# Optimization experiments

Measured on AMD Instinct MI355X. Metric: run time of the kernel, lower is better.

## Reference

```python
import jax, jax.numpy as jnp
import numpy as np


def setup_inputs() -> dict:
    key = jax.random.key(0)
    ks = jax.random.split(key, 7)
    B, C, L, A = 8, 1024, 2048, 128
    x = jax.random.normal(ks[0], (B, C, L), dtype=jnp.float32)
    Wk = jax.random.normal(ks[1], (A, C), dtype=jnp.float32) * (1.0 / np.sqrt(C))
    bk = jax.random.normal(ks[2], (A,), dtype=jnp.float32) * 0.01
    Wq = jax.random.normal(ks[3], (A, C), dtype=jnp.float32) * (1.0 / np.sqrt(C))
    bq = jax.random.normal(ks[4], (A,), dtype=jnp.float32) * 0.01
    Wp = jax.random.normal(ks[5], (C, C), dtype=jnp.float32) * (1.0 / np.sqrt(C))
    bp = jax.random.normal(ks[6], (C,), dtype=jnp.float32) * 0.01
    return {"x": x, "Wk": Wk, "bk": bk, "Wq": Wq, "bq": bq, "Wp": Wp, "bp": bp}


def reference(x, Wk, bk, Wq, bq, Wp, bp):
    # x: [B, C, L]; 1x1 Conv1d == pointwise linear over channel dim
    keys = jnp.einsum('bcl,ac->bal', x, Wk) + bk[None, :, None]      # [B, A, L]
    queries = jnp.einsum('bcl,ac->bal', x, Wq) + bq[None, :, None]   # [B, A, L]
    values = jnp.einsum('bal,bam->blm', keys, queries)               # keys^T @ queries -> [B, L, L]
    seqlen = x.shape[2]
    # NOTE: source uses seqlen ** 1 / 2 which is seqlen/2 due to Python precedence
    attn = jax.nn.softmax(values / (seqlen / 2.0), axis=-1)          # [B, L, L]
    out = jnp.einsum('bcl,blm->bcm', x, attn)                        # x @ attn -> [B, C, L]
    out = jnp.einsum('bcm,dc->bdm', out, Wp) + bp[None, :, None]     # output projection
    return out
```

## Files before the change

kernel.cpp:

```cpp
#include <hip/hip_runtime.h>
#include <hip/hip_bf16.h>

typedef __hip_bfloat16 bf16;
typedef __attribute__((ext_vector_type(8))) short bfrag8;
typedef __attribute__((ext_vector_type(8))) int intx8;
typedef __attribute__((ext_vector_type(4))) float floatx4;


__device__ __forceinline__ unsigned char f2fp8(float f) {
    f = fminf(fmaxf(f, -448.f), 448.f);
    return (unsigned char)(__builtin_amdgcn_cvt_pk_fp8_f32(f, f, 0, false) & 0xFF);
}

__device__ __forceinline__ void async_copy16(const void* g, void* lds) {
    __builtin_amdgcn_global_load_lds(
        (const __attribute__((address_space(1))) unsigned int*)g,
        (__attribute__((address_space(3))) unsigned int*)lds, 16, 0, 0);
}

template<int BIASMODE, int OUTKIND, bool EXPZ, bool MFAST>
__global__ __launch_bounds__(256)
void gemm128(const bf16* __restrict__ Ag, long sAb, int lda,
             const bf16* __restrict__ Bg, long sBb, int ldb,
             void* __restrict__ Cg, long sCb, int ldc,
             const float* __restrict__ scl, const float* __restrict__ b2,
             float* __restrict__ Zp, int K, int logfast)
{
    __shared__ unsigned short As[128 * 64];
    __shared__ unsigned short Bs[128 * 64];

    const int lin = blockIdx.x;
    const int bz  = lin & 7;
    const int s   = lin >> 3;
    const int msk = (1 << logfast) - 1;
    int mT, nT;
    if (MFAST) { mT = s & msk; nT = s >> logfast; }
    else       { nT = s & msk; mT = s >> logfast; }

    const bf16* A  = Ag + (size_t)bz * sAb + (size_t)mT * 128 * lda;
    const bf16* Bp = Bg + (size_t)bz * sBb + (size_t)nT * 128 * ldb;
    const int t = threadIdx.x, wave = t >> 6, lane = t & 63;
    const int qrow = lane & 15, quad = lane >> 4;
    const int wr = (wave >> 1) * 64, wc = (wave & 1) * 64;

    floatx4 acc[4][4] = {};

    for (int k0 = 0; k0 < K; k0 += 64) {
        #pragma unroll
        for (int j = 0; j < 4; ++j) {
            int c = j * 256 + t;
            int r = c >> 3, p = c & 7;
            int g = p ^ (r & 7);
            async_copy16(A + (size_t)r * lda + k0 + g * 8, &As[c * 8]);
        }
        #pragma unroll
        for (int j = 0; j < 4; ++j) {
            int c = j * 256 + t;
            int r = c >> 3, p = c & 7;
            int g = p ^ (r & 7);
            async_copy16(Bp + (size_t)r * ldb + k0 + g * 8, &Bs[c * 8]);
        }
        __syncthreads();

        #pragma unroll
        for (int ks = 0; ks < 2; ++ks) {
            bfrag8 af[4], bfv[4];
            #pragma unroll
            for (int mi = 0; mi < 4; ++mi) {
                int row = wr + mi * 16 + qrow;
                int ck  = ks * 4 + quad;
                af[mi] = *(const bfrag8*)&As[row * 64 + ((ck ^ (row & 7)) * 8)];
            }
            #pragma unroll
            for (int ni = 0; ni < 4; ++ni) {
                int row = wc + ni * 16 + qrow;
                int ck  = ks * 4 + quad;
                bfv[ni] = *(const bfrag8*)&Bs[row * 64 + ((ck ^ (row & 7)) * 8)];
            }
            #pragma unroll
            for (int mi = 0; mi < 4; ++mi)
                #pragma unroll
                for (int ni = 0; ni < 4; ++ni)
                    acc[mi][ni] = __builtin_amdgcn_mfma_f32_16x16x32_bf16(
                        af[mi], bfv[ni], acc[mi][ni], 0, 0, 0);
        }
        __syncthreads();
    }

    const int bmr = mT * 128 + wr, bnc = nT * 128 + wc;
    float zp[4] = {0.f, 0.f, 0.f, 0.f};
    #pragma unroll
    for (int mi = 0; mi < 4; ++mi) {
        #pragma unroll
        for (int ni = 0; ni < 4; ++ni) {
            int col = bnc + ni * 16 + qrow;
            #pragma unroll
            for (int r = 0; r < 4; ++r) {
                int row = bmr + mi * 16 + quad * 4 + r;
                float v = acc[mi][ni][r];
                if (EXPZ) { float e = __expf(v); zp[ni] += e; v = (e - 1.0f) * 4096.0f; }
                if (BIASMODE == 1) v = v * scl[col] + b2[col];
                if (BIASMODE == 2) v += scl[row];
                if (OUTKIND == 1)
                    ((float*)Cg + (size_t)bz * sCb)[(size_t)row * ldc + col] = v;
                else if (OUTKIND == 0)
                    ((bf16*)Cg + (size_t)bz * sCb)[(size_t)row * ldc + col] = __float2bfloat16(v);
                else
                    ((unsigned char*)Cg + (size_t)bz * sCb)[(size_t)row * ldc + col] = f2fp8(v);
            }
        }
    }
    if (EXPZ) {
        #pragma unroll
        for (int ni = 0; ni < 4; ++ni) {
            float tt = zp[ni];
            tt += __shfl_xor(tt, 16, 64);
            tt += __shfl_xor(tt, 32, 64);
            if (quad == 0)
                atomicAdd(&Zp[bz * 2048 + bnc + ni * 16 + qrow], tt);
        }
    }
}

template<int MODE, bool MFAST>
__global__ __launch_bounds__(512, 2)
void gemm_f8(const unsigned char* __restrict__ Ag, long sAb, int lda,
             const unsigned char* __restrict__ Bg, long sBb, int ldb,
             void* __restrict__ Cg, long sCb, int ldc,
             const float* __restrict__ rowb, float os, int K, int logfast)
{
    __shared__ __align__(16) unsigned char smem[131072];

    const int lin = blockIdx.x;
    const int bz  = lin & 7;
    const int s0  = lin >> 3;
    const int msk = (1 << logfast) - 1;
    int mT, nT;
    if (MFAST) { mT = s0 & msk; nT = s0 >> logfast; }
    else       { nT = s0 & msk; mT = s0 >> logfast; }

    const unsigned char* A  = Ag + (size_t)bz * sAb + (size_t)mT * 256 * lda;
    const unsigned char* Bp = Bg + (size_t)bz * sBb + (size_t)nT * 256 * ldb;
    const int t = threadIdx.x, wave = t >> 6, lane = t & 63;
    const int qrow = lane & 15, quad = lane >> 4;
    const int wm = (wave >> 2) * 128;
    const int wn = (wave & 3) * 64;

    floatx4 acc[8][4] = {};

    auto stage_part = [&](int kt, int slot, int part) {
        const int k0 = kt << 7;
        unsigned char* Ad = &smem[slot * 32768];
        unsigned char* Bd = &smem[65536 + slot * 32768];
        #pragma unroll
        for (int j = 0; j < 2; ++j) {
            int c = (part * 2 + j) * 512 + t;
            int r = c >> 3, p = c & 7, g = p ^ (r & 7);
            async_copy16(A + (size_t)r * lda + k0 + g * 16, Ad + c * 16);
        }
        #pragma unroll
        for (int j = 0; j < 2; ++j) {
            int c = (part * 2 + j) * 512 + t;
            int r = c >> 3, p = c & 7, g = p ^ (r & 7);
            async_copy16(Bp + (size_t)r * ldb + k0 + g * 16, Bd + c * 16);
        }
    };

    const int NT = K >> 7;
    stage_part(0, 0, 0);
    stage_part(0, 0, 1);

    for (int kt = 0; kt < NT; ++kt) {
        const int slot = kt & 1;
        const unsigned char* As = &smem[slot * 32768];
        const unsigned char* Bs = &smem[65536 + slot * 32768];

        asm volatile("s_waitcnt vmcnt(0)" ::: "memory");
        __builtin_amdgcn_sched_barrier(0);
        __builtin_amdgcn_s_barrier();
        __builtin_amdgcn_sched_barrier(0);

        intx8 bfr[4];
        #pragma unroll
        for (int ph = 0; ph < 4; ++ph) {
            if (ph == 0) {
                #pragma unroll
                for (int ni = 0; ni < 4; ++ni) {
                    int row = wn + ni * 16 + qrow, sw = row & 7;
                    union { intx8 v; uint4 q[2]; } u;
                    u.q[0] = *(const uint4*)&Bs[row * 128 + (((quad * 2    ) ^ sw) * 16)];
                    u.q[1] = *(const uint4*)&Bs[row * 128 + (((quad * 2 + 1) ^ sw) * 16)];
                    bfr[ni] = u.v;
                }
            }
            intx8 af0, af1;
            {
                int row = wm + (2 * ph) * 16 + qrow, sw = row & 7;
                union { intx8 v; uint4 q[2]; } u;
                u.q[0] = *(const uint4*)&As[row * 128 + (((quad * 2    ) ^ sw) * 16)];
                u.q[1] = *(const uint4*)&As[row * 128 + (((quad * 2 + 1) ^ sw) * 16)];
                af0 = u.v;
            }
            {
                int row = wm + (2 * ph + 1) * 16 + qrow, sw = row & 7;
                union { intx8 v; uint4 q[2]; } u;
                u.q[0] = *(const uint4*)&As[row * 128 + (((quad * 2    ) ^ sw) * 16)];
                u.q[1] = *(const uint4*)&As[row * 128 + (((quad * 2 + 1) ^ sw) * 16)];
                af1 = u.v;
            }
            if (ph < 2 && kt + 1 < NT) stage_part(kt + 1, slot ^ 1, ph);

            __builtin_amdgcn_sched_barrier(0);
            __builtin_amdgcn_s_barrier();
            asm volatile("s_waitcnt lgkmcnt(0)" ::: "memory");
            __builtin_amdgcn_sched_barrier(0);

            __builtin_amdgcn_s_setprio(1);
            #pragma unroll
            for (int ni = 0; ni < 4; ++ni)
                acc[2 * ph][ni] = __builtin_amdgcn_mfma_scale_f32_16x16x128_f8f6f4(
                    af0, bfr[ni], acc[2 * ph][ni], 0, 0, 0, 127, 0, 127);
            #pragma unroll
            for (int ni = 0; ni < 4; ++ni)
                acc[2 * ph + 1][ni] = __builtin_amdgcn_mfma_scale_f32_16x16x128_f8f6f4(
                    af1, bfr[ni], acc[2 * ph + 1][ni], 0, 0, 0, 127, 0, 127);
            __builtin_amdgcn_s_setprio(0);

            __builtin_amdgcn_sched_barrier(0);
            __builtin_amdgcn_s_barrier();
            __builtin_amdgcn_sched_barrier(0);
        }
    }

    const int bmr = mT * 256 + wm, bnc = nT * 256 + wn;
    #pragma unroll
    for (int mi = 0; mi < 8; ++mi) {
        int row0 = bmr + mi * 16 + quad * 4;
        float4 rb4;
        if (MODE == 2) rb4 = *(const float4*)&rowb[bz * 1024 + row0];
        #pragma unroll
        for (int ni = 0; ni < 4; ++ni) {
            int col = bnc + ni * 16 + qrow;
            floatx4 a = acc[mi][ni];
            if (MODE == 2) {
                float* Co = (float*)Cg + (size_t)bz * sCb;
                Co[(size_t)(row0 + 0) * ldc + col] = a[0] * os + rb4.x;
                Co[(size_t)(row0 + 1) * ldc + col] = a[1] * os + rb4.y;
                Co[(size_t)(row0 + 2) * ldc + col] = a[2] * os + rb4.z;
                Co[(size_t)(row0 + 3) * ldc + col] = a[3] * os + rb4.w;
            } else {
                unsigned char* C8 = (unsigned char*)Cg + (size_t)bz * sCb;
                #pragma unroll
                for (int r = 0; r < 4; ++r)
                    C8[(size_t)(row0 + r) * ldc + col] = f2fp8(a[r] * os);
            }
        }
    }
}

__global__ __launch_bounds__(256)
void conv_w(const float* __restrict__ Wk, const float* __restrict__ Wq,
            const float* __restrict__ Wp, bf16* __restrict__ Wkqb,
            unsigned char* __restrict__ Wp8)
{
    int i = blockIdx.x * 256 + threadIdx.x;
    if (i < 32768) {
        const float* src = (i < 16384) ? Wk : Wq;
        int off = (i < 16384) ? i : i - 16384;
        bf16* dst = Wkqb + (size_t)((i < 16384) ? 0 : 131072);
        const float4* sp = (const float4*)src + (size_t)off * 2;
        float4 a = sp[0], b = sp[1];
        union { uint4 u; unsigned short h[8]; } o;
        union { bf16 h; unsigned short u; } cv;
        cv.h = __float2bfloat16(a.x); o.h[0] = cv.u;
        cv.h = __float2bfloat16(a.y); o.h[1] = cv.u;
        cv.h = __float2bfloat16(a.z); o.h[2] = cv.u;
        cv.h = __float2bfloat16(a.w); o.h[3] = cv.u;
        cv.h = __float2bfloat16(b.x); o.h[4] = cv.u;
        cv.h = __float2bfloat16(b.y); o.h[5] = cv.u;
        cv.h = __float2bfloat16(b.z); o.h[6] = cv.u;
        cv.h = __float2bfloat16(b.w); o.h[7] = cv.u;
        ((uint4*)dst)[off] = o.u;
    } else {
        int off = i - 32768;
        const float4* sp = (const float4*)Wp + (size_t)off * 2;
        float4 a = sp[0], b = sp[1];
        unsigned char o[8];
        o[0] = f2fp8(a.x * 2048.f); o[1] = f2fp8(a.y * 2048.f);
        o[2] = f2fp8(a.z * 2048.f); o[3] = f2fp8(a.w * 2048.f);
        o[4] = f2fp8(b.x * 2048.f); o[5] = f2fp8(b.y * 2048.f);
        o[6] = f2fp8(b.z * 2048.f); o[7] = f2fp8(b.w * 2048.f);
        uint2 w;
        w.x = (unsigned int)o[0] | ((unsigned int)o[1] << 8) | ((unsigned int)o[2] << 16) | ((unsigned int)o[3] << 24);
        w.y = (unsigned int)o[4] | ((unsigned int)o[5] << 8) | ((unsigned int)o[6] << 16) | ((unsigned int)o[7] << 24);
        ((uint2*)Wp8)[off] = w;
    }
}

__global__ __launch_bounds__(256)
void conv_x(const float* __restrict__ x, bf16* __restrict__ xt)
{
    const int b = blockIdx.z;
    const int l0 = blockIdx.x * 64, c0 = blockIdx.y * 64;
    const float* xp = x + (size_t)b * 1024 * 2048;
    bf16* xtp = xt + (size_t)b * 2048 * 1024;
    __shared__ unsigned short tile[64][65];
    const int t = threadIdx.x, tr = t >> 4, tc4 = (t & 15) * 4;
    union { bf16 h; unsigned short u; } cv;
    #pragma unroll
    for (int i = 0; i < 4; ++i) {
        int r = i * 16 + tr;
        float4 v = *(const float4*)(xp + (size_t)(c0 + r) * 2048 + l0 + tc4);
        cv.h = __float2bfloat16(v.x); tile[r][tc4]     = cv.u;
        cv.h = __float2bfloat16(v.y); tile[r][tc4 + 1] = cv.u;
        cv.h = __float2bfloat16(v.z); tile[r][tc4 + 2] = cv.u;
        cv.h = __float2bfloat16(v.w); tile[r][tc4 + 3] = cv.u;
    }
    __syncthreads();
    #pragma unroll
    for (int i = 0; i < 4; ++i) {
        int lr = i * 16 + tr;
        union { uint2 u; unsigned short h[4]; } o;
        #pragma unroll
        for (int j = 0; j < 4; ++j) o.h[j] = tile[tc4 + j][lr];
        *(uint2*)(xtp + (size_t)(l0 + lr) * 1024 + c0 + tc4) = o.u;
    }
}

__global__ void prep_bias(const float* __restrict__ bk, const float* __restrict__ bq,
                          float* __restrict__ scl, float* __restrict__ b2, float kscale)
{
    int t = threadIdx.x;
    float s = (t < 128) ? kscale : 1.0f;
    scl[t] = s;
    b2[t] = ((t < 128) ? bk[t] : bq[t - 128]) * s;
}

__global__ __launch_bounds__(256)
void normx(const float* __restrict__ x, const float* __restrict__ Z,
           unsigned char* __restrict__ xs, float* __restrict__ colsum)
{
    const int bc = blockIdx.x;
    const int b  = bc >> 10;
    const int t  = threadIdx.x;
    const float* xp = x + (size_t)bc * 2048 + t * 8;
    const float* zp = Z + b * 2048 + t * 8;
    float4 a = ((const float4*)xp)[0], c4 = ((const float4*)xp)[1];
    float4 z0 = ((const float4*)zp)[0], z1 = ((const float4*)zp)[1];
    float v[8];
    v[0] = a.x  / fmaxf(z0.x, 1e-10f); v[1] = a.y / fmaxf(z0.y, 1e-10f);
    v[2] = a.z  / fmaxf(z0.z, 1e-10f); v[3] = a.w / fmaxf(z0.w, 1e-10f);
    v[4] = c4.x / fmaxf(z1.x, 1e-10f); v[5] = c4.y / fmaxf(z1.y, 1e-10f);
    v[6] = c4.z / fmaxf(z1.z, 1e-10f); v[7] = c4.w / fmaxf(z1.w, 1e-10f);
    float s = 0.f;
    unsigned char o[8];
    #pragma unroll
    for (int j = 0; j < 8; ++j) { s += v[j]; o[j] = f2fp8(v[j] * 65536.f); }
    uint2 w;
    w.x = (unsigned int)o[0] | ((unsigned int)o[1] << 8) | ((unsigned int)o[2] << 16) | ((unsigned int)o[3] << 24);
    w.y = (unsigned int)o[4] | ((unsigned int)o[5] << 8) | ((unsigned int)o[6] << 16) | ((unsigned int)o[7] << 24);
    ((uint2*)(xs + (size_t)bc * 2048))[t] = w;
    #pragma unroll
    for (int off = 32; off >= 1; off >>= 1) s += __shfl_xor(s, off, 64);
    __shared__ float red[4];
    if ((t & 63) == 0) red[t >> 6] = s;
    __syncthreads();
    if (t == 0) colsum[bc] = red[0] + red[1] + red[2] + red[3];
}

__global__ __launch_bounds__(256)
void basek(const float* __restrict__ Wp, const float* __restrict__ colsum,
           const float* __restrict__ bp, float* __restrict__ base)
{
    const int d = blockIdx.x, t = threadIdx.x;
    float4 w = *(const float4*)(Wp + (size_t)d * 1024 + t * 4);
    float pb[8];
    #pragma unroll
    for (int b = 0; b < 8; ++b) {
        float4 cs = *(const float4*)(colsum + b * 1024 + t * 4);
        pb[b] = w.x * cs.x + w.y * cs.y + w.z * cs.z + w.w * cs.w;
    }
    __shared__ float red[8][4];
    #pragma unroll
    for (int b = 0; b < 8; ++b) {
        float s = pb[b];
        #pragma unroll
        for (int off = 32; off >= 1; off >>= 1) s += __shfl_xor(s, off, 64);
        if ((t & 63) == 0) red[b][t >> 6] = s;
    }
    __syncthreads();
    if (t < 8) base[t * 1024 + d] = bp[d] + red[t][0] + red[t][1] + red[t][2] + red[t][3];
}

extern "C" void kernel_launch(void* const* d_in, const int* in_sizes, int n_in,
                              void* d_out, int out_size, void* d_ws, size_t ws_size,
                              hipStream_t stream)
{
    const float* x  = (const float*)d_in[0];
    const float* Wk = (const float*)d_in[1];
    const float* bk = (const float*)d_in[2];
    const float* Wq = (const float*)d_in[3];
    const float* bq = (const float*)d_in[4];
    const float* Wp = (const float*)d_in[5];
    const float* bp = (const float*)d_in[6];
    float* out = (float*)d_out;

    const float kscale = 2.0f / 2048.0f;

    bf16* xt   = (bf16*)d_ws;
    bf16* KQt  = xt + (size_t)8 * 2048 * 1024;
    bf16* Wkqb = KQt + (size_t)8 * 2048 * 256;
    unsigned char* Wp8 = (unsigned char*)(Wkqb + (size_t)256 * 1024);
    unsigned char* St8 = Wp8 + (size_t)1048576;
    unsigned char* xs8 = St8 + (size_t)8 * 2048 * 2048;
    float* Z      = (float*)(xs8 + (size_t)8 * 1024 * 2048);
    float* colsum = Z + 8 * 2048;
    float* base   = colsum + 8 * 1024;
    float* scl    = base + 8 * 1024;
    float* b2     = scl + 256;
    unsigned char* Dlt = (unsigned char*)xt;

    dim3 blk(256, 1, 1);
    dim3 blk512(512, 1, 1);

    prep_bias<<<dim3(1), blk, 0, stream>>>(bk, bq, scl, b2, kscale);
    conv_w<<<dim3(640), blk, 0, stream>>>(Wk, Wq, Wp, Wkqb, Wp8);
    conv_x<<<dim3(32, 16, 8), blk, 0, stream>>>(x, xt);

    gemm128<1, 0, false, false><<<dim3(8 * 16 * 2), blk, 0, stream>>>(
        xt, 2048L * 1024, 1024,  Wkqb, 0, 1024,
        KQt, 2048L * 256, 256,  scl, b2, nullptr, 1024, 1);

    hipMemsetAsync(Z, 0, (size_t)8 * 2048 * sizeof(float), stream);

    gemm128<0, 2, true, false><<<dim3(8 * 16 * 16), blk, 0, stream>>>(
        KQt + 128, 2048L * 256, 256,  KQt, 2048L * 256, 256,
        St8, 2048L * 2048, 2048,  nullptr, nullptr, Z, 128, 4);

    normx<<<dim3(8 * 1024), blk, 0, stream>>>(x, Z, xs8, colsum);
    basek<<<dim3(1024), blk, 0, stream>>>(Wp, colsum, bp, base);

    gemm_f8<0, false><<<dim3(8 * 8 * 4), blk512, 0, stream>>>(
        St8, 2048L * 2048, 2048,  xs8, 1024L * 2048, 2048,
        Dlt, 2048L * 1024, 1024,  nullptr, 0.0009765625f, 2048, 2);

    gemm_f8<2, true><<<dim3(8 * 4 * 8), blk512, 0, stream>>>(
        Wp8, 0, 1024,  Dlt, 2048L * 1024, 1024,
        out, 1024L * 2048, 2048,  base, 1.862645149230957e-9f, 1024, 2);
}
```

Before: 260.2 us.

## Replace score GEMM with dedicated 256x256-tile single-stage kernel with fused exp

Adds a specialized kernel for the keys^T·queries score GEMM (K=128) that uses 512 threads and 256x256 output tiles. The whole K extent is loaded into LDS in one step with an XOR swizzle, and the MFMAs run without a K loop. Exp, the fp8 conversion and the column-sum atomics are fused into the epilogue. The goal is to cut per-block overhead and redundant operand loads compared with the generic 128-tile kernel. The cost is heavy register use (128 accumulators per thread) and 128KB of LDS per block, which limits occupancy.

Measured after the change: 261.8 us. No clear change (+0.6%).

```diff
diff --git a/kernel.cpp b/kernel.cpp
--- a/kernel.cpp
+++ b/kernel.cpp
@@ -119,6 +119,96 @@
             if (quad == 0)
                 atomicAdd(&Zp[bz * 2048 + bnc + ni * 16 + qrow], tt);
         }
+    }
+}
+
+__global__ __launch_bounds__(512, 2)
+void gemm_s3(const bf16* __restrict__ Ag, long sAb, int lda,
+             const bf16* __restrict__ Bg, long sBb, int ldb,
+             unsigned char* __restrict__ Cg, long sCb, int ldc,
+             float* __restrict__ Zp)
+{
+    __shared__ __align__(16) unsigned char smem[131072];
+
+    const int lin = blockIdx.x;
+    const int bz  = lin & 7;
+    const int s0  = lin >> 3;
+    const int nT  = s0 & 7, mT = s0 >> 3;
+
+    const bf16* A  = Ag + (size_t)bz * sAb + (size_t)mT * 256 * lda;
+    const bf16* Bp = Bg + (size_t)bz * sBb + (size_t)nT * 256 * ldb;
+    const int t = threadIdx.x, wave = t >> 6, lane = t & 63;
+    const int qrow = lane & 15, quad = lane >> 4;
+    const int wm = (wave >> 2) * 128;
+    const int wn = (wave & 3) * 64;
+
+    unsigned char* As = smem;
+    unsigned char* Bs = smem + 65536;
+
+    #pragma unroll
+    for (int j = 0; j < 8; ++j) {
+        int c = j * 512 + t;
+        int r = c >> 4, p = c & 15;
+        int g = (p & 8) | ((p & 7) ^ (r & 7));
+        async_copy16(A + (size_t)r * lda + g * 8, As + c * 16);
+    }
+    #pragma unroll
+    for (int j = 0; j < 8; ++j) {
+        int c = j * 512 + t;
+        int r = c >> 4, p = c & 15;
+        int g = (p & 8) | ((p & 7) ^ (r & 7));
+        async_copy16(Bp + (size_t)r * ldb + g * 8, Bs + c * 16);
+    }
+    asm volatile("s_waitcnt vmcnt(0)" ::: "memory");
+    __builtin_amdgcn_s_barrier();
+
+    floatx4 acc[8][4] = {};
+    #pragma unroll
+    for (int ks = 0; ks < 4; ++ks) {
+        const int ck = ks * 4 + quad;
+        bfrag8 bfv[4];
+        #pragma unroll
+        for (int ni = 0; ni < 4; ++ni) {
+            int row = wn + ni * 16 + qrow;
+            int ph  = (ck & 8) | ((ck & 7) ^ (row & 7));
+            bfv[ni] = *(const bfrag8*)&Bs[row * 256 + ph * 16];
+        }
+        #pragma unroll
+        for (int mi = 0; mi < 8; ++mi) {
+            int row = wm + mi * 16 + qrow;
+            int ph  = (ck & 8) | ((ck & 7) ^ (row & 7));
+            bfrag8 af = *(const bfrag8*)&As[row * 256 + ph * 16];
+            #pragma unroll
+            for (int ni = 0; ni < 4; ++ni)
+                acc[mi][ni] = __builtin_amdgcn_mfma_f32_16x16x32_bf16(
+                    af, bfv[ni], acc[mi][ni], 0, 0, 0);
+        }
+    }
+
+    const int bmr = mT * 256 + wm, bnc = nT * 256 + wn;
+    unsigned char* C8 = Cg + (size_t)bz * sCb;
+    float zp[4] = {0.f, 0.f, 0.f, 0.f};
+    #pragma unroll
+    for (int mi = 0; mi < 8; ++mi) {
+        #pragma unroll
+        for (int ni = 0; ni < 4; ++ni) {
+            int col = bnc + ni * 16 + qrow;
+            #pragma unroll
+            for (int r = 0; r < 4; ++r) {
+                int row = bmr + mi * 16 + quad * 4 + r;
+                float e = __expf(acc[mi][ni][r]);
+                zp[ni] += e;
+                C8[(size_t)row * ldc + col] = f2fp8((e - 1.0f) * 4096.0f);
+            }
+        }
+    }
+    #pragma unroll
+    for (int ni = 0; ni < 4; ++ni) {
+        float tt = zp[ni];
+        tt += __shfl_xor(tt, 16, 64);
+        tt += __shfl_xor(tt, 32, 64);
+        if (quad == 0)
+            atomicAdd(&Zp[bz * 2048 + bnc + ni * 16 + qrow], tt);
     }
 }
 
@@ -433,9 +523,9 @@
 
     hipMemsetAsync(Z, 0, (size_t)8 * 2048 * sizeof(float), stream);
 
-    gemm128<0, 2, true, false><<<dim3(8 * 16 * 16), blk, 0, stream>>>(
+    gemm_s3<<<dim3(8 * 8 * 8), blk512, 0, stream>>>(
         KQt + 128, 2048L * 256, 256,  KQt, 2048L * 256, 256,
-        St8, 2048L * 2048, 2048,  nullptr, nullptr, Z, 128, 4);
+        St8, 2048L * 2048, 2048,  Z);
 
     normx<<<dim3(8 * 1024), blk, 0, stream>>>(x, Z, xs8, colsum);
     basek<<<dim3(1024), blk, 0, stream>>>(Wp, colsum, bp, base);
```
